# Kernel tuning notes

Hardware: AMD Instinct MI355X
Metric: run time of the kernel (lower is better)

## Reference

```python
import jax, jax.numpy as jnp
import numpy as np

N0, N1, N2 = 10000, 40000, 160000
E1, E2 = 240000, 960000
C_IN, C_MID, C_OUT = 64, 32, 16  # up_convs = [64, 32, 16]


def _basis(pseudo):
    """Open quadratic B-spline basis, kernel_size=3, degree=2, dim=2.
    With kernel_size-degree == 1, v = pseudo in [0,1) and all 3 basis fns per dim
    are active with fixed indices 0..2, so the 2-D product gives 9 weights/edge."""
    t = pseudo  # [E, 2]
    b = jnp.stack([0.5 * (1.0 - t) ** 2, -t * t + t + 0.5, 0.5 * t * t], axis=-1)  # [E,2,3]
    return (b[:, 0, :, None] * b[:, 1, None, :]).reshape(t.shape[0], 9)  # [E, 9]


def _spline_conv(x, src, dst, basis, W, R, b, n):
    # x: [N, Cin], W: [9, Cin, Cout], R: [Cin, Cout], b: [Cout]
    xs = x[src]  # [E, Cin] gather
    m = basis[:, 0:1] * (xs @ W[0])
    for k in range(1, 9):  # fixed small kernel loop; avoids [E,9,Cout] blowup
        m = m + basis[:, k:k + 1] * (xs @ W[k])
    agg = jax.ops.segment_sum(m, dst, num_segments=n)  # aggr='add'
    return agg + x @ R + b


def _up_level(x_coarse, unpool, edge, pseudo, skip, W1, R1, b1, W2, R2, b2):
    n = unpool.shape[0]
    x = x_coarse[unpool]          # MeshUnpool: copy coarse features to fine verts
    basis = _basis(pseudo)
    src, dst = edge[0], edge[1]
    h = jax.nn.relu(_spline_conv(x, src, dst, basis, W1, R1, b1, n))
    h = jnp.concatenate([h, skip], axis=1)  # [n, 2*Cout] == Cin
    h = jax.nn.relu(_spline_conv(h, src, dst, basis, W1, R1, b1, n))  # conv1 reused
    h = jax.nn.relu(_spline_conv(h, src, dst, basis, W2, R2, b2, n))
    return h


def setup_inputs() -> dict:
    key = jax.random.key(0)
    ks = jax.random.split(key, 24)
    s = 0.05
    inp = {
        'x0': jax.random.normal(ks[0], (N0, C_IN), jnp.float32),
        'unpool1': jax.random.randint(ks[1], (N1,), 0, N0),
        'edge1': jax.random.randint(ks[2], (2, E1), 0, N1),
        'pseudo1': jax.random.uniform(ks[3], (E1, 2), jnp.float32),
        'skip1': jax.random.normal(ks[4], (N1, C_MID), jnp.float32),
        'unpool2': jax.random.randint(ks[5], (N2,), 0, N1),
        'edge2': jax.random.randint(ks[6], (2, E2), 0, N2),
        'pseudo2': jax.random.uniform(ks[7], (E2, 2), jnp.float32),
        'skip2': jax.random.normal(ks[8], (N2, C_OUT), jnp.float32),
        # level 1 (UpConv 64 -> 32)
        'W1a': jax.random.normal(ks[9], (9, C_IN, C_MID), jnp.float32) * s,
        'R1a': jax.random.normal(ks[10], (C_IN, C_MID), jnp.float32) * s,
        'b1a': jax.random.normal(ks[11], (C_MID,), jnp.float32) * s,
        'W2a': jax.random.normal(ks[12], (9, C_MID, C_MID), jnp.float32) * s,
        'R2a': jax.random.normal(ks[13], (C_MID, C_MID), jnp.float32) * s,
        'b2a': jax.random.normal(ks[14], (C_MID,), jnp.float32) * s,
        # level 2 (UpConv 32 -> 16)
        'W1b': jax.random.normal(ks[15], (9, C_MID, C_OUT), jnp.float32) * s,
        'R1b': jax.random.normal(ks[16], (C_MID, C_OUT), jnp.float32) * s,
        'b1b': jax.random.normal(ks[17], (C_OUT,), jnp.float32) * s,
        'W2b': jax.random.normal(ks[18], (9, C_OUT, C_OUT), jnp.float32) * s,
        'R2b': jax.random.normal(ks[19], (C_OUT, C_OUT), jnp.float32) * s,
        'b2b': jax.random.normal(ks[20], (C_OUT,), jnp.float32) * s,
    }
    return inp


def reference(x0, unpool1, edge1, pseudo1, skip1, unpool2, edge2, pseudo2, skip2,
              W1a, R1a, b1a, W2a, R2a, b2a, W1b, R1b, b1b, W2b, R2b, b2b):
    h1 = _up_level(x0, unpool1, edge1, pseudo1, skip1, W1a, R1a, b1a, W2a, R2a, b2a)
    h2 = _up_level(h1, unpool2, edge2, pseudo2, skip2, W1b, R1b, b1b, W2b, R2b, b2b)
    return h2
```

## Files before the change

kernel.cpp:

```cpp
#include <hip/hip_runtime.h>
#include <stdint.h>

typedef __bf16 bf16x8 __attribute__((ext_vector_type(8)));
typedef __bf16 bf16x4 __attribute__((ext_vector_type(4)));
typedef float  f32x4  __attribute__((ext_vector_type(4)));

__global__ void k_up_b2b(const uint4* __restrict__ xin, const int* __restrict__ up,
                         uint4* __restrict__ xout, int N, int rowU4) {
  int i = blockIdx.x * 256 + threadIdx.x;
  if (i >= N * rowU4) return;
  int n = i / rowU4, j = i - n * rowU4;
  xout[i] = xin[(size_t)up[n] * rowU4 + j];
}

__device__ __forceinline__ void d_pack(int o,
    const float* W1a, const float* R1a, const float* W2a, const float* R2a,
    const float* W1b, const float* R1b, const float* W2b, const float* R2b,
    __bf16* BpA, __bf16* BpB, __bf16* BpC, __bf16* BpD) {
  const float *W, *R; __bf16* Bp; int Cin, Cout;
  if (o < 20480)      { W = W1a; R = R1a; Bp = BpA; Cin = 64; Cout = 32; }
  else if (o < 30720) { W = W2a; R = R2a; Bp = BpB; Cin = 32; Cout = 32; o -= 20480; }
  else if (o < 35840) { W = W1b; R = R1b; Bp = BpC; Cin = 32; Cout = 16; o -= 30720; }
  else if (o < 38400) { W = W2b; R = R2b; Bp = BpD; Cin = 16; Cout = 16; o -= 35840; }
  else return;
  int CT = Cout / 16;
  int j = o & 7, lane = (o >> 3) & 63, tile = o >> 9;
  int ct = tile % CT, kc = tile / CT;
  int k = kc * 32 + ((lane >> 4) * 8) + j;
  int n = ct * 16 + (lane & 15);
  float v;
  if (k < 9 * Cin) { int k9 = k / Cin, cin = k - k9 * Cin; v = W[(k9 * Cin + cin) * Cout + n]; }
  else             { v = R[(k - 9 * Cin) * Cout + n]; }
  Bp[o] = (__bf16)v;
}

__device__ __forceinline__ void d_bhist(int b, int t, const int* dst, int E,
                                        int* bcnt, int nbk) {
  __shared__ int h[256];
  h[t] = 0;
  __syncthreads();
  int e0 = b * 2048 + t * 8;
  if (e0 + 8 <= E) {
    int4 a = *reinterpret_cast<const int4*>(dst + e0);
    int4 c = *reinterpret_cast<const int4*>(dst + e0 + 4);
    atomicAdd(&h[a.x >> 10], 1); atomicAdd(&h[a.y >> 10], 1);
    atomicAdd(&h[a.z >> 10], 1); atomicAdd(&h[a.w >> 10], 1);
    atomicAdd(&h[c.x >> 10], 1); atomicAdd(&h[c.y >> 10], 1);
    atomicAdd(&h[c.z >> 10], 1); atomicAdd(&h[c.w >> 10], 1);
  } else {
    for (int j = 0; j < 8; ++j)
      if (e0 + j < E) atomicAdd(&h[dst[e0 + j] >> 10], 1);
  }
  __syncthreads();
  if (t < nbk && h[t]) atomicAdd(&bcnt[t], h[t]);
}

__global__ __launch_bounds__(256) void k_prologue(
    const float* __restrict__ W1a, const float* __restrict__ R1a,
    const float* __restrict__ W2a, const float* __restrict__ R2a,
    const float* __restrict__ W1b, const float* __restrict__ R1b,
    const float* __restrict__ W2b, const float* __restrict__ R2b,
    __bf16* __restrict__ BpA, __bf16* __restrict__ BpB,
    __bf16* __restrict__ BpC, __bf16* __restrict__ BpD,
    const float4* __restrict__ x0, const int* __restrict__ up1, __bf16* __restrict__ x1,
    const int* __restrict__ dst1, int E1, int* __restrict__ bcnt1, int nbk1,
    const int* __restrict__ dst2, int E2, int* __restrict__ bcnt2, int nbk2,
    int N1) {
  int b = blockIdx.x, t = threadIdx.x;
  if (b < 150) {
    d_pack(b * 256 + t, W1a, R1a, W2a, R2a, W1b, R1b, W2b, R2b, BpA, BpB, BpC, BpD);
  } else if (b < 2650) {
    int i = (b - 150) * 256 + t;
    if (i < N1 * 16) {
      int n = i >> 4, j = i & 15;
      float4 v = x0[(size_t)up1[n] * 16 + j];
      bf16x4 o = {(__bf16)v.x, (__bf16)v.y, (__bf16)v.z, (__bf16)v.w};
      *reinterpret_cast<bf16x4*>(x1 + (size_t)n * 64 + j * 4) = o;
    }
  } else if (b < 2768) {
    d_bhist(b - 2650, t, dst1, E1, bcnt1, nbk1);
  } else {
    d_bhist(b - 2768, t, dst2, E2, bcnt2, nbk2);
  }
}

__global__ void k_bscan_dual(const int* __restrict__ bcnt1, int nbk1, int E1,
                             int* __restrict__ bstart1, int* __restrict__ bcur1,
                             const int* __restrict__ bcnt2, int nbk2, int E2,
                             int* __restrict__ bstart2, int* __restrict__ bcur2) {
  const int* bcnt; int nbk, E; int *bstart, *bcur;
  if (blockIdx.x == 0) { bcnt = bcnt1; nbk = nbk1; E = E1; bstart = bstart1; bcur = bcur1; }
  else                 { bcnt = bcnt2; nbk = nbk2; E = E2; bstart = bstart2; bcur = bcur2; }
  __shared__ int wsum[4];
  int t = threadIdx.x, lane = t & 63, w = t >> 6;
  int v = (t < nbk) ? bcnt[t] : 0;
  int x = v;
  #pragma unroll
  for (int o = 1; o < 64; o <<= 1) { int y = __shfl_up(x, o, 64); if (lane >= o) x += y; }
  if (lane == 63) wsum[w] = x;
  __syncthreads();
  int wpre = 0;
  #pragma unroll
  for (int k = 0; k < 4; ++k) if (k < w) wpre += wsum[k];
  int excl = wpre + x - v;
  if (t < nbk) { bstart[t] = excl; bcur[t] = excl; }
  if (t == 0) bstart[nbk] = E;
}

__device__ __forceinline__ void d_bpart(int b, int t, const int* src, const int* dst,
                                        const float2* pse, int E, int* bcur,
                                        uint2* ebuf, int nbk) {
  __shared__ int h[256];
  __shared__ int base[256];
  h[t] = 0;
  __syncthreads();
  int e0 = b * 2048 + t * 8;
  int d[8], rank[8];
  bool full = (e0 + 8 <= E);
  if (full) {
    int4 a = *reinterpret_cast<const int4*>(dst + e0);
    int4 c = *reinterpret_cast<const int4*>(dst + e0 + 4);
    d[0] = a.x; d[1] = a.y; d[2] = a.z; d[3] = a.w;
    d[4] = c.x; d[5] = c.y; d[6] = c.z; d[7] = c.w;
    #pragma unroll
    for (int j = 0; j < 8; ++j) rank[j] = atomicAdd(&h[d[j] >> 10], 1);
  } else {
    #pragma unroll
    for (int j = 0; j < 8; ++j)
      if (e0 + j < E) { d[j] = dst[e0 + j]; rank[j] = atomicAdd(&h[d[j] >> 10], 1); }
  }
  __syncthreads();
  if (t < nbk && h[t]) base[t] = atomicAdd(&bcur[t], h[t]);
  __syncthreads();
  if (full) {
    int4 a = *reinterpret_cast<const int4*>(src + e0);
    int4 c = *reinterpret_cast<const int4*>(src + e0 + 4);
    int s[8] = {a.x, a.y, a.z, a.w, c.x, c.y, c.z, c.w};
    float2 p[8];
    #pragma unroll
    for (int j = 0; j < 8; ++j) p[j] = pse[e0 + j];
    #pragma unroll
    for (int j = 0; j < 8; ++j) {
      int bkt = d[j] >> 10, dloc = d[j] & 1023;
      union { uint u; _Float16 hh[2]; } cv;
      cv.hh[0] = (_Float16)p[j].x; cv.hh[1] = (_Float16)p[j].y;
      ebuf[base[bkt] + rank[j]] = make_uint2((uint)s[j] | ((uint)dloc << 18), cv.u);
    }
  } else {
    #pragma unroll
    for (int j = 0; j < 8; ++j) {
      if (e0 + j >= E) continue;
      int bkt = d[j] >> 10, dloc = d[j] & 1023;
      float2 p = pse[e0 + j];
      union { uint u; _Float16 hh[2]; } cv;
      cv.hh[0] = (_Float16)p.x; cv.hh[1] = (_Float16)p.y;
      ebuf[base[bkt] + rank[j]] = make_uint2((uint)src[e0 + j] | ((uint)dloc << 18), cv.u);
    }
  }
}

__global__ __launch_bounds__(256) void k_bpart_dual(
    const int* __restrict__ src1, const int* __restrict__ dst1, const float2* __restrict__ pse1,
    int E1, int* __restrict__ bcur1, uint2* __restrict__ ebuf1, int nbk1, int NB1,
    const int* __restrict__ src2, const int* __restrict__ dst2, const float2* __restrict__ pse2,
    int E2, int* __restrict__ bcur2, uint2* __restrict__ ebuf2, int nbk2) {
  int b = blockIdx.x, t = threadIdx.x;
  if (b < NB1) d_bpart(b, t, src1, dst1, pse1, E1, bcur1, ebuf1, nbk1);
  else         d_bpart(b - NB1, t, src2, dst2, pse2, E2, bcur2, ebuf2, nbk2);
}

__device__ __forceinline__ void d_bcsr(int b, int t, const int* bstart, const uint2* ebuf,
                                       uint2* epk, int* off, int N, int E, int nbk) {
  __shared__ int cnt[1024];
  __shared__ int excl[1024];
  __shared__ int cur[1024];
  __shared__ int wsum[4];
  int e0 = bstart[b], e1 = bstart[b + 1];
  #pragma unroll
  for (int k = 0; k < 4; ++k) { cnt[t * 4 + k] = 0; cur[t * 4 + k] = 0; }
  __syncthreads();
  for (int i = e0 + t; i < e1; i += 256)
    atomicAdd(&cnt[(ebuf[i].x >> 18) & 1023], 1);
  __syncthreads();
  int lane = t & 63, w = t >> 6;
  int i0 = t * 4;
  int c0 = cnt[i0], c1 = cnt[i0 + 1], c2 = cnt[i0 + 2], c3 = cnt[i0 + 3];
  int s = c0 + c1 + c2 + c3, x = s;
  #pragma unroll
  for (int o = 1; o < 64; o <<= 1) { int y = __shfl_up(x, o, 64); if (lane >= o) x += y; }
  if (lane == 63) wsum[w] = x;
  __syncthreads();
  int wpre = 0;
  #pragma unroll
  for (int k = 0; k < 4; ++k) if (k < w) wpre += wsum[k];
  int ex = wpre + x - s;
  excl[i0] = ex; excl[i0 + 1] = ex + c0; excl[i0 + 2] = ex + c0 + c1; excl[i0 + 3] = ex + c0 + c1 + c2;
  int dg0 = b * 1024;
  int exv[4] = {ex, ex + c0, ex + c0 + c1, ex + c0 + c1 + c2};
  #pragma unroll
  for (int k = 0; k < 4; ++k) {
    int d = dg0 + i0 + k;
    if (d < N) off[d] = e0 + exv[k];
  }
  __syncthreads();
  for (int i = e0 + t; i < e1; i += 256) {
    uint2 r = ebuf[i];
    int dloc = (r.x >> 18) & 1023;
    int rk = atomicAdd(&cur[dloc], 1);
    epk[e0 + excl[dloc] + rk] = make_uint2(r.x & 0x3FFFFu, r.y);
  }
  if (b == nbk - 1 && t == 0) off[N] = E;
}

__global__ __launch_bounds__(256) void k_bcsr_dual(
    const int* __restrict__ bstart1, const uint2* __restrict__ ebuf1, uint2* __restrict__ epk1,
    int* __restrict__ off1, int N1, int E1, int nbk1,
    const int* __restrict__ bstart2, const uint2* __restrict__ ebuf2, uint2* __restrict__ epk2,
    int* __restrict__ off2, int N2, int E2, int nbk2) {
  int b = blockIdx.x, t = threadIdx.x;
  if (b < nbk1) d_bcsr(b, t, bstart1, ebuf1, epk1, off1, N1, E1, nbk1);
  else          d_bcsr(b - nbk1, t, bstart2, ebuf2, epk2, off2, N2, E2, nbk2);
}

template<int Cin, int Cout, bool OUTF32, bool HAS_SKIP>
__global__ __launch_bounds__(256, 4) void k_conv(const int* __restrict__ off,
                        const uint2* __restrict__ epk,
                        const __bf16* __restrict__ X, const __bf16* __restrict__ Bp,
                        const float* __restrict__ bias, const float* __restrict__ skip,
                        void* __restrict__ outv, int N, int outStride) {
  constexpr int LPD = Cin / 4;
  constexpr int DPB = 256 / LPD;
  constexpr int K   = 10 * Cin;
  constexpr int KP2 = K + 8;
  constexpr int NT  = DPB / 16;
  constexpr int KC  = K / 32;
  constexpr int CT  = Cout / 16;
  constexpr int UNITS = NT * CT;

  __shared__ __bf16 As[DPB * KP2];

  int t = threadIdx.x;
  int g = t / LPD, sub = t % LPD;
  int d = blockIdx.x * DPB + g;

  float acc[9][4];
  #pragma unroll
  for (int k = 0; k < 9; ++k)
    #pragma unroll
    for (int v = 0; v < 4; ++v) acc[k][v] = 0.f;
  bf16x4 xd = {};

  if (d < N) {
    xd = *reinterpret_cast<const bf16x4*>(X + (size_t)d * Cin + sub * 4);
    int b0 = off[d], b1 = off[d + 1];
    int i = b0;
    for (; i + 4 <= b1; i += 4) {
      uint2 e0 = epk[i], e1 = epk[i + 1], e2 = epk[i + 2], e3 = epk[i + 3];
      bf16x4 xf0 = *reinterpret_cast<const bf16x4*>(X + (size_t)e0.x * Cin + sub * 4);
      bf16x4 xf1 = *reinterpret_cast<const bf16x4*>(X + (size_t)e1.x * Cin + sub * 4);
      bf16x4 xf2 = *reinterpret_cast<const bf16x4*>(X + (size_t)e2.x * Cin + sub * 4);
      bf16x4 xf3 = *reinterpret_cast<const bf16x4*>(X + (size_t)e3.x * Cin + sub * 4);
      uint ps[4] = {e0.y, e1.y, e2.y, e3.y};
      bf16x4 xfs[4] = {xf0, xf1, xf2, xf3};
      #pragma unroll
      for (int c = 0; c < 4; ++c) {
        union { uint u; _Float16 h[2]; } cv; cv.u = ps[c];
        float t0 = (float)cv.h[0], t1 = (float)cv.h[1];
        float u0 = 1.f - t0;
        float wi[3] = {0.5f * u0 * u0, -t0 * t0 + t0 + 0.5f, 0.5f * t0 * t0};
        float u1 = 1.f - t1;
        float wj[3] = {0.5f * u1 * u1, -t1 * t1 + t1 + 0.5f, 0.5f * t1 * t1};
        float xfv[4];
        #pragma unroll
        for (int v = 0; v < 4; ++v) xfv[v] = (float)xfs[c][v];
        #pragma unroll
        for (int ki = 0; ki < 3; ++ki)
          #pragma unroll
          for (int kj = 0; kj < 3; ++kj) {
            float w = wi[ki] * wj[kj];
            #pragma unroll
            for (int v = 0; v < 4; ++v)
              acc[ki * 3 + kj][v] += w * xfv[v];
          }
      }
    }
    for (; i < b1; ++i) {
      uint2 ep = epk[i];
      bf16x4 xf = *reinterpret_cast<const bf16x4*>(X + (size_t)ep.x * Cin + sub * 4);
      union { uint u; _Float16 h[2]; } cv; cv.u = ep.y;
      float t0 = (float)cv.h[0], t1 = (float)cv.h[1];
      float u0 = 1.f - t0;
      float wi[3] = {0.5f * u0 * u0, -t0 * t0 + t0 + 0.5f, 0.5f * t0 * t0};
      float u1 = 1.f - t1;
      float wj[3] = {0.5f * u1 * u1, -t1 * t1 + t1 + 0.5f, 0.5f * t1 * t1};
      float xfv[4];
      #pragma unroll
      for (int v = 0; v < 4; ++v) xfv[v] = (float)xf[v];
      #pragma unroll
      for (int ki = 0; ki < 3; ++ki)
        #pragma unroll
        for (int kj = 0; kj < 3; ++kj) {
          float w = wi[ki] * wj[kj];
          #pragma unroll
          for (int v = 0; v < 4; ++v)
            acc[ki * 3 + kj][v] += w * xfv[v];
        }
    }
  }

  __bf16* row = As + (size_t)g * KP2;
  #pragma unroll
  for (int k = 0; k < 9; ++k) {
    bf16x4 tmp;
    #pragma unroll
    for (int v = 0; v < 4; ++v) tmp[v] = (__bf16)acc[k][v];
    *reinterpret_cast<bf16x4*>(row + k * Cin + sub * 4) = tmp;
  }
  *reinterpret_cast<bf16x4*>(row + 9 * Cin + sub * 4) = xd;
  __syncthreads();

  int lane = t & 63, wave = t >> 6;
  int c15 = lane & 15, q = lane >> 4;
  for (int u = wave; u < UNITS; u += 4) {
    int tile = u / CT, ct = u - tile * CT;
    const __bf16* arow = As + (size_t)(tile * 16 + c15) * KP2 + q * 8;
    f32x4 a4 = {0.f, 0.f, 0.f, 0.f};
    #pragma unroll
    for (int kc = 0; kc < KC; ++kc) {
      bf16x8 a = *reinterpret_cast<const bf16x8*>(arow + kc * 32);
      bf16x8 b = *reinterpret_cast<const bf16x8*>(Bp + ((size_t)(kc * CT + ct) * 64 + lane) * 8);
      a4 = __builtin_amdgcn_mfma_f32_16x16x32_bf16(a, b, a4, 0, 0, 0);
    }
    int cout = ct * 16 + c15;
    float bb = bias[cout];
    #pragma unroll
    for (int r = 0; r < 4; ++r) {
      int m = q * 4 + r;
      int dd = blockIdx.x * DPB + tile * 16 + m;
      if (dd < N) {
        float vv = fmaxf(a4[r] + bb, 0.f);
        if constexpr (OUTF32)
          ((float*)outv)[(size_t)dd * outStride + cout] = vv;
        else
          ((__bf16*)outv)[(size_t)dd * outStride + cout] = (__bf16)vv;
        if constexpr (HAS_SKIP) {
          float sv = skip[(size_t)dd * Cout + cout];
          ((__bf16*)outv)[(size_t)dd * outStride + Cout + cout] = (__bf16)sv;
        }
      }
    }
  }
}

extern "C" void kernel_launch(void* const* d_in, const int* in_sizes, int n_in,
                              void* d_out, int out_size, void* d_ws, size_t ws_size,
                              hipStream_t stream) {
  const float* x0      = (const float*)d_in[0];
  const int*   up1     = (const int*)d_in[1];
  const int*   edge1   = (const int*)d_in[2];
  const float* pseudo1 = (const float*)d_in[3];
  const float* skip1   = (const float*)d_in[4];
  const int*   up2     = (const int*)d_in[5];
  const int*   edge2   = (const int*)d_in[6];
  const float* pseudo2 = (const float*)d_in[7];
  const float* skip2   = (const float*)d_in[8];
  const float* W1a = (const float*)d_in[9];
  const float* R1a = (const float*)d_in[10];
  const float* b1a = (const float*)d_in[11];
  const float* W2a = (const float*)d_in[12];
  const float* R2a = (const float*)d_in[13];
  const float* b2a = (const float*)d_in[14];
  const float* W1b = (const float*)d_in[15];
  const float* R1b = (const float*)d_in[16];
  const float* b1b = (const float*)d_in[17];
  const float* W2b = (const float*)d_in[18];
  const float* R2b = (const float*)d_in[19];
  const float* b2b = (const float*)d_in[20];

  const int N1 = 40000, N2 = 160000, E1 = 240000, E2 = 960000;
  const int NBK1 = 40, NBK2 = 157;
  const int NB1 = (E1 + 2047) / 2048;
  const int NB2 = (E2 + 2047) / 2048;

  char* ws = (char*)d_ws;
  __bf16* x1     = (__bf16*)(ws);
  __bf16* xcat1  = (__bf16*)(ws +  5120000);
  __bf16* x3     = (__bf16*)(ws + 10240000);
  __bf16* h1     = (__bf16*)(ws + 12800000);
  __bf16* x2     = (__bf16*)(ws + 15360000);
  __bf16* xcat2  = (__bf16*)(ws + 25600000);
  __bf16* x6     = (__bf16*)(ws + 35840000);
  int*   off1    = (int*)(ws + 40960000);
  uint2* ebuf1   = (uint2*)(ws + 41120016);
  uint2* epk1    = (uint2*)(ws + 43040016);
  int*   off2    = (int*)(ws + 44960016);
  uint2* ebuf2   = (uint2*)(ws + 45600032);
  uint2* epk2    = (uint2*)(ws + 53280032);
  int*   bcnt12  = (int*)(ws + 60960032);
  int*   bstart1 = (int*)(ws + 60962080);
  int*   bcur1   = (int*)(ws + 60962336);
  int*   bstart2 = (int*)(ws + 60962592);
  int*   bcur2   = (int*)(ws + 60963616);
  __bf16* BpA    = (__bf16*)(ws + 60964640);
  __bf16* BpB    = (__bf16*)(ws + 61005600);
  __bf16* BpC    = (__bf16*)(ws + 61026080);
  __bf16* BpD    = (__bf16*)(ws + 61036320);
  int* bcnt1 = bcnt12, *bcnt2 = bcnt12 + 256;

  hipMemsetAsync(bcnt12, 0, 512 * 4, stream);

  k_prologue<<<150 + 2500 + NB1 + NB2, 256, 0, stream>>>(
      W1a, R1a, W2a, R2a, W1b, R1b, W2b, R2b, BpA, BpB, BpC, BpD,
      (const float4*)x0, up1, x1,
      edge1 + E1, E1, bcnt1, NBK1,
      edge2 + E2, E2, bcnt2, NBK2, N1);

  k_bscan_dual<<<2, 256, 0, stream>>>(bcnt1, NBK1, E1, bstart1, bcur1,
                                      bcnt2, NBK2, E2, bstart2, bcur2);

  k_bpart_dual<<<NB1 + NB2, 256, 0, stream>>>(
      edge1, edge1 + E1, (const float2*)pseudo1, E1, bcur1, ebuf1, NBK1, NB1,
      edge2, edge2 + E2, (const float2*)pseudo2, E2, bcur2, ebuf2, NBK2);

  k_bcsr_dual<<<NBK1 + NBK2, 256, 0, stream>>>(
      bstart1, ebuf1, epk1, off1, N1, E1, NBK1,
      bstart2, ebuf2, epk2, off2, N2, E2, NBK2);

  k_conv<64, 32, false, true><<<N1 / 16, 256, 0, stream>>>(off1, epk1, x1, BpA, b1a, skip1, xcat1, N1, 64);
  k_conv<64, 32, false, false><<<N1 / 16, 256, 0, stream>>>(off1, epk1, xcat1, BpA, b1a, nullptr, x3, N1, 32);
  k_conv<32, 32, false, false><<<N1 / 32, 256, 0, stream>>>(off1, epk1, x3, BpB, b2a, nullptr, h1, N1, 32);

  k_up_b2b<<<N2 * 4 / 256, 256, 0, stream>>>((const uint4*)h1, up2, (uint4*)x2, N2, 4);

  k_conv<32, 16, false, true><<<N2 / 32, 256, 0, stream>>>(off2, epk2, x2, BpC, b1b, skip2, xcat2, N2, 32);
  k_conv<32, 16, false, false><<<N2 / 32, 256, 0, stream>>>(off2, epk2, xcat2, BpC, b1b, nullptr, x6, N2, 16);
  k_conv<16, 16, true, false><<<N2 / 64, 256, 0, stream>>>(off2, epk2, x6, BpD, b2b, nullptr, d_out, N2, 16);
}
```

Before: 318.2 us.

## Fold mesh unpool into edge source indices instead of materializing unpooled features

Removes the explicit unpool gather kernels (x1 and x2 materialization). Edge source indices are remapped through the unpool table during partitioning and stored as a second packed edge list. The first conv of each level reads the coarse features directly, remapping the destination row via up[]. This saves writing and re-reading 40k×64 and 160k×32 intermediate arrays. In exchange it adds an extra 16-bit buffer and a second packed edge array in the preprocessing path. Occupancy launch bounds are also raised for Cin<=32 kernels.

```diff
diff --git a/kernel.cpp b/kernel.cpp
--- a/kernel.cpp
+++ b/kernel.cpp
@@ -4,14 +4,6 @@
 typedef __bf16 bf16x8 __attribute__((ext_vector_type(8)));
 typedef __bf16 bf16x4 __attribute__((ext_vector_type(4)));
 typedef float  f32x4  __attribute__((ext_vector_type(4)));
-
-__global__ void k_up_b2b(const uint4* __restrict__ xin, const int* __restrict__ up,
-                         uint4* __restrict__ xout, int N, int rowU4) {
-  int i = blockIdx.x * 256 + threadIdx.x;
-  if (i >= N * rowU4) return;
-  int n = i / rowU4, j = i - n * rowU4;
-  xout[i] = xin[(size_t)up[n] * rowU4 + j];
-}
 
 __device__ __forceinline__ void d_pack(int o,
     const float* W1a, const float* R1a, const float* W2a, const float* R2a,
@@ -62,25 +54,23 @@
     const float* __restrict__ W2b, const float* __restrict__ R2b,
     __bf16* __restrict__ BpA, __bf16* __restrict__ BpB,
     __bf16* __restrict__ BpC, __bf16* __restrict__ BpD,
-    const float4* __restrict__ x0, const int* __restrict__ up1, __bf16* __restrict__ x1,
+    const float4* __restrict__ x0, __bf16* __restrict__ x0bf,
     const int* __restrict__ dst1, int E1, int* __restrict__ bcnt1, int nbk1,
-    const int* __restrict__ dst2, int E2, int* __restrict__ bcnt2, int nbk2,
-    int N1) {
+    const int* __restrict__ dst2, int E2, int* __restrict__ bcnt2, int nbk2) {
   int b = blockIdx.x, t = threadIdx.x;
   if (b < 150) {
     d_pack(b * 256 + t, W1a, R1a, W2a, R2a, W1b, R1b, W2b, R2b, BpA, BpB, BpC, BpD);
-  } else if (b < 2650) {
+  } else if (b < 775) {
     int i = (b - 150) * 256 + t;
-    if (i < N1 * 16) {
-      int n = i >> 4, j = i & 15;
-      float4 v = x0[(size_t)up1[n] * 16 + j];
+    if (i < 160000) {
+      float4 v = x0[i];
       bf16x4 o = {(__bf16)v.x, (__bf16)v.y, (__bf16)v.z, (__bf16)v.w};
-      *reinterpret_cast<bf16x4*>(x1 + (size_t)n * 64 + j * 4) = o;
-    }
-  } else if (b < 2768) {
-    d_bhist(b - 2650, t, dst1, E1, bcnt1, nbk1);
+      *reinterpret_cast<bf16x4*>(x0bf + (size_t)i * 4) = o;
+    }
+  } else if (b < 893) {
+    d_bhist(b - 775, t, dst1, E1, bcnt1, nbk1);
   } else {
-    d_bhist(b - 2768, t, dst2, E2, bcnt2, nbk2);
+    d_bhist(b - 893, t, dst2, E2, bcnt2, nbk2);
   }
 }
 
@@ -108,8 +98,8 @@
 }
 
 __device__ __forceinline__ void d_bpart(int b, int t, const int* src, const int* dst,
-                                        const float2* pse, int E, int* bcur,
-                                        uint2* ebuf, int nbk) {
+                                        const float2* pse, const int* up, int E, int* bcur,
+                                        uint2* ebuf, uint16_t* rbuf, int nbk) {
   __shared__ int h[256];
   __shared__ int base[256];
   h[t] = 0;
@@ -136,41 +126,52 @@
     int4 a = *reinterpret_cast<const int4*>(src + e0);
     int4 c = *reinterpret_cast<const int4*>(src + e0 + 4);
     int s[8] = {a.x, a.y, a.z, a.w, c.x, c.y, c.z, c.w};
+    int u[8];
+    #pragma unroll
+    for (int j = 0; j < 8; ++j) u[j] = up[s[j]];
     float2 p[8];
     #pragma unroll
     for (int j = 0; j < 8; ++j) p[j] = pse[e0 + j];
     #pragma unroll
     for (int j = 0; j < 8; ++j) {
       int bkt = d[j] >> 10, dloc = d[j] & 1023;
-      union { uint u; _Float16 hh[2]; } cv;
+      union { uint uu; _Float16 hh[2]; } cv;
       cv.hh[0] = (_Float16)p[j].x; cv.hh[1] = (_Float16)p[j].y;
-      ebuf[base[bkt] + rank[j]] = make_uint2((uint)s[j] | ((uint)dloc << 18), cv.u);
+      int pos = base[bkt] + rank[j];
+      ebuf[pos] = make_uint2((uint)s[j] | ((uint)dloc << 18), cv.uu);
+      rbuf[pos] = (uint16_t)u[j];
     }
   } else {
     #pragma unroll
     for (int j = 0; j < 8; ++j) {
       if (e0 + j >= E) continue;
       int bkt = d[j] >> 10, dloc = d[j] & 1023;
+      int sj = src[e0 + j];
       float2 p = pse[e0 + j];
-      union { uint u; _Float16 hh[2]; } cv;
+      union { uint uu; _Float16 hh[2]; } cv;
       cv.hh[0] = (_Float16)p.x; cv.hh[1] = (_Float16)p.y;
-      ebuf[base[bkt] + rank[j]] = make_uint2((uint)src[e0 + j] | ((uint)dloc << 18), cv.u);
+      int pos = base[bkt] + rank[j];
+      ebuf[pos] = make_uint2((uint)sj | ((uint)dloc << 18), cv.uu);
+      rbuf[pos] = (uint16_t)up[sj];
     }
   }
 }
 
 __global__ __launch_bounds__(256) void k_bpart_dual(
     const int* __restrict__ src1, const int* __restrict__ dst1, const float2* __restrict__ pse1,
-    int E1, int* __restrict__ bcur1, uint2* __restrict__ ebuf1, int nbk1, int NB1,
+    const int* __restrict__ up1, int E1, int* __restrict__ bcur1,
+    uint2* __restrict__ ebuf1, uint16_t* __restrict__ rbuf1, int nbk1, int NB1,
     const int* __restrict__ src2, const int* __restrict__ dst2, const float2* __restrict__ pse2,
-    int E2, int* __restrict__ bcur2, uint2* __restrict__ ebuf2, int nbk2) {
+    const int* __restrict__ up2, int E2, int* __restrict__ bcur2,
+    uint2* __restrict__ ebuf2, uint16_t* __restrict__ rbuf2, int nbk2) {
   int b = blockIdx.x, t = threadIdx.x;
-  if (b < NB1) d_bpart(b, t, src1, dst1, pse1, E1, bcur1, ebuf1, nbk1);
-  else         d_bpart(b - NB1, t, src2, dst2, pse2, E2, bcur2, ebuf2, nbk2);
+  if (b < NB1) d_bpart(b, t, src1, dst1, pse1, up1, E1, bcur1, ebuf1, rbuf1, nbk1);
+  else         d_bpart(b - NB1, t, src2, dst2, pse2, up2, E2, bcur2, ebuf2, rbuf2, nbk2);
 }
 
 __device__ __forceinline__ void d_bcsr(int b, int t, const int* bstart, const uint2* ebuf,
-                                       uint2* epk, int* off, int N, int E, int nbk) {
+                                       const uint16_t* rbuf, uint2* epk, uint2* epkR,
+                                       int* off, int N, int E, int nbk) {
   __shared__ int cnt[1024];
   __shared__ int excl[1024];
   __shared__ int cur[1024];
@@ -205,28 +206,35 @@
   __syncthreads();
   for (int i = e0 + t; i < e1; i += 256) {
     uint2 r = ebuf[i];
+    uint rs = rbuf[i];
     int dloc = (r.x >> 18) & 1023;
     int rk = atomicAdd(&cur[dloc], 1);
-    epk[e0 + excl[dloc] + rk] = make_uint2(r.x & 0x3FFFFu, r.y);
+    int pos = e0 + excl[dloc] + rk;
+    epk[pos]  = make_uint2(r.x & 0x3FFFFu, r.y);
+    epkR[pos] = make_uint2(rs, r.y);
   }
   if (b == nbk - 1 && t == 0) off[N] = E;
 }
 
 __global__ __launch_bounds__(256) void k_bcsr_dual(
-    const int* __restrict__ bstart1, const uint2* __restrict__ ebuf1, uint2* __restrict__ epk1,
+    const int* __restrict__ bstart1, const uint2* __restrict__ ebuf1,
+    const uint16_t* __restrict__ rbuf1, uint2* __restrict__ epk1, uint2* __restrict__ epkR1,
     int* __restrict__ off1, int N1, int E1, int nbk1,
-    const int* __restrict__ bstart2, const uint2* __restrict__ ebuf2, uint2* __restrict__ epk2,
+    const int* __restrict__ bstart2, const uint2* __restrict__ ebuf2,
+    const uint16_t* __restrict__ rbuf2, uint2* __restrict__ epk2, uint2* __restrict__ epkR2,
     int* __restrict__ off2, int N2, int E2, int nbk2) {
   int b = blockIdx.x, t = threadIdx.x;
-  if (b < nbk1) d_bcsr(b, t, bstart1, ebuf1, epk1, off1, N1, E1, nbk1);
-  else          d_bcsr(b - nbk1, t, bstart2, ebuf2, epk2, off2, N2, E2, nbk2);
-}
-
-template<int Cin, int Cout, bool OUTF32, bool HAS_SKIP>
-__global__ __launch_bounds__(256, 4) void k_conv(const int* __restrict__ off,
+  if (b < nbk1) d_bcsr(b, t, bstart1, ebuf1, rbuf1, epk1, epkR1, off1, N1, E1, nbk1);
+  else          d_bcsr(b - nbk1, t, bstart2, ebuf2, rbuf2, epk2, epkR2, off2, N2, E2, nbk2);
+}
+
+template<int Cin, int Cout, bool OUTF32, bool HAS_SKIP, bool REMAP>
+__global__ __launch_bounds__(256, (Cin <= 32 ? 8 : 4)) void k_conv(
+                        const int* __restrict__ off,
                         const uint2* __restrict__ epk,
                         const __bf16* __restrict__ X, const __bf16* __restrict__ Bp,
                         const float* __restrict__ bias, const float* __restrict__ skip,
+                        const int* __restrict__ up,
                         void* __restrict__ outv, int N, int outStride) {
   constexpr int LPD = Cin / 4;
   constexpr int DPB = 256 / LPD;
@@ -251,7 +259,9 @@
   bf16x4 xd = {};
 
   if (d < N) {
-    xd = *reinterpret_cast<const bf16x4*>(X + (size_t)d * Cin + sub * 4);
+    int dsrc = d;
+    if constexpr (REMAP) dsrc = up[d];
+    xd = *reinterpret_cast<const bf16x4*>(X + (size_t)dsrc * Cin + sub * 4);
     int b0 = off[d], b1 = off[d + 1];
     int i = b0;
     for (; i + 4 <= b1; i += 4) {
@@ -383,56 +393,57 @@
   const int NB2 = (E2 + 2047) / 2048;
 
   char* ws = (char*)d_ws;
-  __bf16* x1     = (__bf16*)(ws);
-  __bf16* xcat1  = (__bf16*)(ws +  5120000);
-  __bf16* x3     = (__bf16*)(ws + 10240000);
-  __bf16* h1     = (__bf16*)(ws + 12800000);
-  __bf16* x2     = (__bf16*)(ws + 15360000);
-  __bf16* xcat2  = (__bf16*)(ws + 25600000);
-  __bf16* x6     = (__bf16*)(ws + 35840000);
-  int*   off1    = (int*)(ws + 40960000);
-  uint2* ebuf1   = (uint2*)(ws + 41120016);
-  uint2* epk1    = (uint2*)(ws + 43040016);
-  int*   off2    = (int*)(ws + 44960016);
-  uint2* ebuf2   = (uint2*)(ws + 45600032);
-  uint2* epk2    = (uint2*)(ws + 53280032);
-  int*   bcnt12  = (int*)(ws + 60960032);
-  int*   bstart1 = (int*)(ws + 60962080);
-  int*   bcur1   = (int*)(ws + 60962336);
-  int*   bstart2 = (int*)(ws + 60962592);
-  int*   bcur2   = (int*)(ws + 60963616);
-  __bf16* BpA    = (__bf16*)(ws + 60964640);
-  __bf16* BpB    = (__bf16*)(ws + 61005600);
-  __bf16* BpC    = (__bf16*)(ws + 61026080);
-  __bf16* BpD    = (__bf16*)(ws + 61036320);
+  __bf16* x0bf   = (__bf16*)(ws);
+  __bf16* xcat1  = (__bf16*)(ws +  1280000);
+  __bf16* x3     = (__bf16*)(ws +  6400000);
+  __bf16* h1     = (__bf16*)(ws +  8960000);
+  __bf16* xcat2  = (__bf16*)(ws + 11520000);
+  __bf16* x6     = (__bf16*)(ws + 21760000);
+  int*   off1    = (int*)(ws + 26880000);
+  int*   off2    = (int*)(ws + 27040016);
+  uint2* ebuf1   = (uint2*)(ws + 27680032);
+  uint2* epk1    = (uint2*)(ws + 29600032);
+  uint2* epkR1   = (uint2*)(ws + 31520032);
+  uint16_t* rbuf1 = (uint16_t*)(ws + 33440032);
+  uint2* ebuf2   = (uint2*)(ws + 33920032);
+  uint2* epk2    = (uint2*)(ws + 41600032);
+  uint2* epkR2   = (uint2*)(ws + 49280032);
+  uint16_t* rbuf2 = (uint16_t*)(ws + 56960032);
+  int*   bcnt12  = (int*)(ws + 58880032);
+  int*   bstart1 = (int*)(ws + 58882080);
+  int*   bcur1   = (int*)(ws + 58882336);
+  int*   bstart2 = (int*)(ws + 58882592);
+  int*   bcur2   = (int*)(ws + 58883616);
+  __bf16* BpA    = (__bf16*)(ws + 58884640);
+  __bf16* BpB    = (__bf16*)(ws + 58925600);
+  __bf16* BpC    = (__bf16*)(ws + 58946080);
+  __bf16* BpD    = (__bf16*)(ws + 58956320);
   int* bcnt1 = bcnt12, *bcnt2 = bcnt12 + 256;
 
   hipMemsetAsync(bcnt12, 0, 512 * 4, stream);
 
-  k_prologue<<<150 + 2500 + NB1 + NB2, 256, 0, stream>>>(
+  k_prologue<<<150 + 625 + NB1 + NB2, 256, 0, stream>>>(
       W1a, R1a, W2a, R2a, W1b, R1b, W2b, R2b, BpA, BpB, BpC, BpD,
-      (const float4*)x0, up1, x1,
+      (const float4*)x0, x0bf,
       edge1 + E1, E1, bcnt1, NBK1,
-      edge2 + E2, E2, bcnt2, NBK2, N1);
+      edge2 + E2, E2, bcnt2, NBK2);
 
   k_bscan_dual<<<2, 256, 0, stream>>>(bcnt1, NBK1, E1, bstart1, bcur1,
                                       bcnt2, NBK2, E2, bstart2, bcur2);
 
   k_bpart_dual<<<NB1 + NB2, 256, 0, stream>>>(
-      edge1, edge1 + E1, (const float2*)pseudo1, E1, bcur1, ebuf1, NBK1, NB1,
-      edge2, edge2 + E2, (const float2*)pseudo2, E2, bcur2, ebuf2, NBK2);
+      edge1, edge1 + E1, (const float2*)pseudo1, up1, E1, bcur1, ebuf1, rbuf1, NBK1, NB1,
+      edge2, edge2 + E2, (const float2*)pseudo2, up2, E2, bcur2, ebuf2, rbuf2, NBK2);
 
   k_bcsr_dual<<<NBK1 + NBK2, 256, 0, stream>>>(
-      bstart1, ebuf1, epk1, off1, N1, E1, NBK1,
-      bstart2, ebuf2, epk2, off2, N2, E2, NBK2);
-
-  k_conv<64, 32, false, true><<<N1 / 16, 256, 0, stream>>>(off1, epk1, x1, BpA, b1a, skip1, xcat1, N1, 64);
-  k_conv<64, 32, false, false><<<N1 / 16, 256, 0, stream>>>(off1, epk1, xcat1, BpA, b1a, nullptr, x3, N1, 32);
-  k_conv<32, 32, false, false><<<N1 / 32, 256, 0, stream>>>(off1, epk1, x3, BpB, b2a, nullptr, h1, N1, 32);
-
-  k_up_b2b<<<N2 * 4 / 256, 256, 0, stream>>>((const uint4*)h1, up2, (uint4*)x2, N2, 4);
-
-  k_conv<32, 16, false, true><<<N2 / 32, 256, 0, stream>>>(off2, epk2, x2, BpC, b1b, skip2, xcat2, N2, 32);
-  k_conv<32, 16, false, false><<<N2 / 32, 256, 0, stream>>>(off2, epk2, xcat2, BpC, b1b, nullptr, x6, N2, 16);
-  k_conv<16, 16, true, false><<<N2 / 64, 256, 0, stream>>>(off2, epk2, x6, BpD, b2b, nullptr, d_out, N2, 16);
-}
+      bstart1, ebuf1, rbuf1, epk1, epkR1, off1, N1, E1, NBK1,
+      bstart2, ebuf2, rbuf2, epk2, epkR2, off2, N2, E2, NBK2);
+
+  k_conv<64, 32, false, true,  true ><<<N1 / 16, 256, 0, stream>>>(off1, epkR1, x0bf, BpA, b1a, skip1, up1, xcat1, N1, 64);
+  k_conv<64, 32, false, false, false><<<N1 / 16, 256, 0, stream>>>(off1, epk1, xcat1, BpA, b1a, nullptr, nullptr, x3, N1, 32);
+  k_conv<32, 32, false, false, false><<<N1 / 32, 256, 0, stream>>>(off1, epk1, x3, BpB, b2a, nullptr, nullptr, h1, N1, 32);
+
+  k_conv<32, 16, false, true,  true ><<<N2 / 32, 256, 0, stream>>>(off2, epkR2, h1, BpC, b1b, skip2, up2, xcat2, N2, 32);
+  k_conv<32, 16, false, false, false><<<N2 / 32, 256, 0, stream>>>(off2, epk2, xcat2, BpC, b1b, nullptr, nullptr, x6, N2, 16);
+  k_conv<16, 16, true,  false, false><<<N2 / 64, 256, 0, stream>>>(off2, epk2, x6, BpD, b2b, nullptr, nullptr, d_out, N2, 16);
+}
```

Measured after the change: 322.1 us. About the same (+1.2%).
